# Optimization experiments

Hardware: AMD Instinct MI355X
Metric: run time of the kernel (lower is better)

Reference implementation:

```python
import jax, jax.numpy as jnp
import numpy as np

IN_F = 11008   # named 'in_features' in the module but used as the OUTPUT dim of F.linear
OUT_F = 4096   # named 'out_features' but is x's feature (input) dim
GROUP = 64


def dequantize_q40(w, s):
    """w: int8 (IN_F*OUT_F/GROUP/2, GROUP) packed nibbles; s: fp16 (IN_F*OUT_F/GROUP,).
    Matches torch: MSB = w >> 4 (arithmetic), LSB = w << 4 >> 4 (sign-extended low nibble).
    """
    msb = (w >> 4).astype(jnp.float16)                      # arithmetic shift on int8
    lsb = ((w & 15) - ((w & 8) << 1)).astype(jnp.float16)   # sign-extend low 4 bits to [-8, 7]
    q = jnp.concatenate([msb, lsb], axis=1).reshape(-1, GROUP)  # (n_groups, GROUP)
    fpval = (q * s[:, None]).astype(jnp.float16)
    return fpval.reshape(IN_F, OUT_F)


def setup_inputs() -> dict:
    key = jax.random.key(0)
    k1, k2, k3 = jax.random.split(key, 3)
    x = jax.random.normal(k1, (4, 2048, OUT_F), dtype=jnp.float16)
    n_rows = IN_F * OUT_F // GROUP // 2
    w = jax.random.randint(k2, (n_rows, GROUP), -128, 128, dtype=jnp.int32).astype(jnp.int8)
    s = (jax.random.uniform(k3, (IN_F * OUT_F // GROUP,), dtype=jnp.float32) * 0.02 + 0.001).astype(jnp.float16)
    return {"x": x, "w": w, "s": s}


def reference(x, w, s):
    # F.linear(x, deq) with deq of shape (IN_F, OUT_F): y = x @ deq.T
    deq = dequantize_q40(w, s)  # (IN_F, OUT_F) fp16
    return jnp.einsum('bsk,ok->bso', x, deq)  # (4, 2048, IN_F)
```

## Files before the change

kernel.cpp:

```cpp
#include <hip/hip_runtime.h>
#include <stdint.h>

#define M_DIM 8192
#define K_DIM 4096
#define N_DIM 11008

#define BM 128
#define BN 128
#define BK 64


typedef __attribute__((ext_vector_type(8))) _Float16 half8;
typedef __attribute__((ext_vector_type(4))) _Float16 half4;
typedef __attribute__((ext_vector_type(4))) float floatx4;

#define SWZ(row, col) ((col) ^ (((row) & 7) << 3))

__global__ __launch_bounds__(256) void dequant_q40(const int* __restrict__ w,
                                                   const float* __restrict__ s,
                                                   _Float16* __restrict__ deq) {
    int t = blockIdx.x * 256 + threadIdx.x;
    int r = t >> 3;
    int j = (t & 7) * 8;
    const int* wp = w + (size_t)r * 64 + j;
    int4 p0 = *(const int4*)(wp);
    int4 p1 = *(const int4*)(wp + 4);
    float sm = s[2 * r];
    float sl = s[2 * r + 1];
    int n = r >> 5, u = r & 31;
    _Float16* dm = deq + (size_t)n * K_DIM + u * 128 + j;
    int v[8] = {p0.x, p0.y, p0.z, p0.w, p1.x, p1.y, p1.z, p1.w};
    half8 vm, vl;
#pragma unroll
    for (int i = 0; i < 8; ++i) {
        int b = v[i];
        vm[i] = (_Float16)((float)(b >> 4) * sm);
        vl[i] = (_Float16)((float)((b << 28) >> 28) * sl);
    }
    *(half8*)dm = vm;
    *(half8*)(dm + 64) = vl;
}

__global__ __launch_bounds__(256, 2) void gemm_f16_bt(const float* __restrict__ A,
                                                      const _Float16* __restrict__ B,
                                                      float* __restrict__ C) {
    __shared__ _Float16 As[BM * BK];
    __shared__ _Float16 Bs[BN * BK];

    const int tid  = threadIdx.x;
    const int lane = tid & 63;
    const int wave = tid >> 6;
    const int wm = (wave >> 1) * 64;
    const int wn = (wave & 1) * 64;
    const int m0 = blockIdx.y * BM;
    const int n0 = blockIdx.x * BN;

    floatx4 acc[4][4] = {};
    const int lrow = lane & 15;
    const int quad = lane >> 4;
    const int kxor = (lrow & 7) << 3;

    for (int kk = 0; kk < K_DIM; kk += BK) {
        float4 av[8];
#pragma unroll
        for (int i = 0; i < 8; ++i) {
            int flat = i * 256 + tid;
            int row = flat >> 4;
            int col = (flat & 15) * 4;
            av[i] = *(const float4*)(A + (size_t)(m0 + row) * K_DIM + kk + col);
        }
        half8 bv[4];
#pragma unroll
        for (int i = 0; i < 4; ++i) {
            int flat = i * 256 + tid;
            int row = flat >> 3;
            int col = (flat & 7) * 8;
            bv[i] = *(const half8*)(B + (size_t)(n0 + row) * K_DIM + kk + col);
        }
        __syncthreads();
#pragma unroll
        for (int i = 0; i < 8; ++i) {
            int flat = i * 256 + tid;
            int row = flat >> 4;
            int col = (flat & 15) * 4;
            half4 a16;
            a16[0] = (_Float16)av[i].x;
            a16[1] = (_Float16)av[i].y;
            a16[2] = (_Float16)av[i].z;
            a16[3] = (_Float16)av[i].w;
            *(half4*)(As + row * BK + SWZ(row, col)) = a16;
        }
#pragma unroll
        for (int i = 0; i < 4; ++i) {
            int flat = i * 256 + tid;
            int row = flat >> 3;
            int col = (flat & 7) * 8;
            *(half8*)(Bs + row * BK + SWZ(row, col)) = bv[i];
        }
        __syncthreads();

#pragma unroll
        for (int ks = 0; ks < BK; ks += 32) {
            int koff = (ks + quad * 8) ^ kxor;
            half8 af[4], bf[4];
#pragma unroll
            for (int im = 0; im < 4; ++im)
                af[im] = *(const half8*)(As + (wm + im * 16 + lrow) * BK + koff);
#pragma unroll
            for (int in_ = 0; in_ < 4; ++in_)
                bf[in_] = *(const half8*)(Bs + (wn + in_ * 16 + lrow) * BK + koff);
#pragma unroll
            for (int im = 0; im < 4; ++im)
#pragma unroll
                for (int in_ = 0; in_ < 4; ++in_)
                    acc[im][in_] = __builtin_amdgcn_mfma_f32_16x16x32_f16(
                        af[im], bf[in_], acc[im][in_], 0, 0, 0);
        }
    }

#pragma unroll
    for (int im = 0; im < 4; ++im) {
#pragma unroll
        for (int in_ = 0; in_ < 4; ++in_) {
            int col = n0 + wn + in_ * 16 + lrow;
#pragma unroll
            for (int r = 0; r < 4; ++r) {
                int row = m0 + wm + im * 16 + quad * 4 + r;
                C[(size_t)row * N_DIM + col] = acc[im][in_][r];
            }
        }
    }
}

__global__ __launch_bounds__(256, 2) void gemm_fused(const float* __restrict__ A,
                                                     const int* __restrict__ W,
                                                     const float* __restrict__ S,
                                                     float* __restrict__ C) {
    __shared__ _Float16 As[BM * BK];
    __shared__ _Float16 Bs[BN * BK];

    const int tid  = threadIdx.x;
    const int lane = tid & 63;
    const int wave = tid >> 6;
    const int wm = (wave >> 1) * 64;
    const int wn = (wave & 1) * 64;
    const int m0 = blockIdx.y * BM;
    const int n0 = blockIdx.x * BN;

    floatx4 acc[4][4] = {};
    const int lrow = lane & 15;
    const int quad = lane >> 4;
    const int kxor = (lrow & 7) << 3;

    const int nn = tid >> 1;
    const int bh = (tid & 1) * 32;

    for (int kk = 0; kk < K_DIM; kk += BK) {
        float4 av[8];
#pragma unroll
        for (int i = 0; i < 8; ++i) {
            int flat = i * 256 + tid;
            int row = flat >> 4;
            int col = (flat & 15) * 4;
            av[i] = *(const float4*)(A + (size_t)(m0 + row) * K_DIM + kk + col);
        }
        int t64 = kk >> 6;
        int u = t64 >> 1;
        const int* wr = W + ((size_t)(n0 + nn) * 32 + u) * 64 + bh;
        float sc = S[(size_t)(n0 + nn) * 64 + t64];
        bool sel_lsb = (t64 & 1);
        half8 bq[4];
#pragma unroll
        for (int i8 = 0; i8 < 4; ++i8) {
            int4 pa = *(const int4*)(wr + i8 * 8);
            int4 pb = *(const int4*)(wr + i8 * 8 + 4);
            int vv[8] = {pa.x, pa.y, pa.z, pa.w, pb.x, pb.y, pb.z, pb.w};
#pragma unroll
            for (int q = 0; q < 8; ++q) {
                int b = vv[q];
                int qq = sel_lsb ? ((b << 28) >> 28) : (b >> 4);
                bq[i8][q] = (_Float16)((float)qq * sc);
            }
        }
        __syncthreads();
#pragma unroll
        for (int i = 0; i < 8; ++i) {
            int flat = i * 256 + tid;
            int row = flat >> 4;
            int col = (flat & 15) * 4;
            half4 a16;
            a16[0] = (_Float16)av[i].x;
            a16[1] = (_Float16)av[i].y;
            a16[2] = (_Float16)av[i].z;
            a16[3] = (_Float16)av[i].w;
            *(half4*)(As + row * BK + SWZ(row, col)) = a16;
        }
#pragma unroll
        for (int i8 = 0; i8 < 4; ++i8)
            *(half8*)(Bs + nn * BK + SWZ(nn, bh + i8 * 8)) = bq[i8];
        __syncthreads();

#pragma unroll
        for (int ks = 0; ks < BK; ks += 32) {
            int koff = (ks + quad * 8) ^ kxor;
            half8 af[4], bf[4];
#pragma unroll
            for (int im = 0; im < 4; ++im)
                af[im] = *(const half8*)(As + (wm + im * 16 + lrow) * BK + koff);
#pragma unroll
            for (int in_ = 0; in_ < 4; ++in_)
                bf[in_] = *(const half8*)(Bs + (wn + in_ * 16 + lrow) * BK + koff);
#pragma unroll
            for (int im = 0; im < 4; ++im)
#pragma unroll
                for (int in_ = 0; in_ < 4; ++in_)
                    acc[im][in_] = __builtin_amdgcn_mfma_f32_16x16x32_f16(
                        af[im], bf[in_], acc[im][in_], 0, 0, 0);
        }
    }

#pragma unroll
    for (int im = 0; im < 4; ++im) {
#pragma unroll
        for (int in_ = 0; in_ < 4; ++in_) {
            int col = n0 + wn + in_ * 16 + lrow;
#pragma unroll
            for (int r = 0; r < 4; ++r) {
                int row = m0 + wm + im * 16 + quad * 4 + r;
                C[(size_t)row * N_DIM + col] = acc[im][in_][r];
            }
        }
    }
}

extern "C" void kernel_launch(void* const* d_in, const int* in_sizes, int n_in,
                              void* d_out, int out_size, void* d_ws, size_t ws_size,
                              hipStream_t stream) {
    const float* x = (const float*)d_in[0];
    const int*   w = (const int*)d_in[1];
    const float* s = (const float*)d_in[2];
    float*     out = (float*)d_out;

    const size_t deq_bytes = (size_t)N_DIM * K_DIM * sizeof(_Float16);
    dim3 grid(N_DIM / BN, M_DIM / BM);

    if (ws_size >= deq_bytes) {
        _Float16* deq = (_Float16*)d_ws;
        dequant_q40<<<11008, 256, 0, stream>>>(w, s, deq);
        gemm_f16_bt<<<grid, 256, 0, stream>>>(x, deq, out);
    } else {
        gemm_fused<<<grid, 256, 0, stream>>>(x, w, s, out);
    }
}
```

Measured before the change: 1.581 ms.

## Pre-convert activations to fp16 and load GEMM tiles directly into LDS

Measured after the change: 1.324 ms. 16.3% less time.

```diff
diff --git a/kernel.cpp b/kernel.cpp
--- a/kernel.cpp
+++ b/kernel.cpp
@@ -15,6 +15,11 @@
 typedef __attribute__((ext_vector_type(4))) float floatx4;
 
 #define SWZ(row, col) ((col) ^ (((row) & 7) << 3))
+
+#define GLD_LDS16(gp, lp)                                                     \
+    __builtin_amdgcn_global_load_lds(                                         \
+        (const __attribute__((address_space(1))) uint32_t*)(gp),              \
+        (__attribute__((address_space(3))) uint32_t*)(lp), 16, 0, 0)
 
 __global__ __launch_bounds__(256) void dequant_q40(const int* __restrict__ w,
                                                    const float* __restrict__ s,
@@ -41,6 +46,94 @@
     *(half8*)(dm + 64) = vl;
 }
 
+__global__ __launch_bounds__(256) void conv_a16(const float* __restrict__ A,
+                                                _Float16* __restrict__ A16) {
+    size_t t = (size_t)blockIdx.x * 256 + threadIdx.x;
+    const float* p = A + t * 8;
+    float4 v0 = *(const float4*)(p);
+    float4 v1 = *(const float4*)(p + 4);
+    half8 h;
+    h[0] = (_Float16)v0.x; h[1] = (_Float16)v0.y;
+    h[2] = (_Float16)v0.z; h[3] = (_Float16)v0.w;
+    h[4] = (_Float16)v1.x; h[5] = (_Float16)v1.y;
+    h[6] = (_Float16)v1.z; h[7] = (_Float16)v1.w;
+    *(half8*)(A16 + t * 8) = h;
+}
+
+__global__ __launch_bounds__(256, 2) void gemm_lds16(const _Float16* __restrict__ A,
+                                                     const _Float16* __restrict__ B,
+                                                     float* __restrict__ C) {
+    __shared__ _Float16 As[BM * BK];
+    __shared__ _Float16 Bs[BN * BK];
+
+    const int tid  = threadIdx.x;
+    const int lane = tid & 63;
+    const int wave = tid >> 6;
+    const int wm = (wave >> 1) * 64;
+    const int wn = (wave & 1) * 64;
+
+    const int nwg_per_xcd = (N_DIM / BN) * (M_DIM / BM) / 8;
+    int bid = blockIdx.x;
+    int swz = (bid & 7) * nwg_per_xcd + (bid >> 3);
+    const int n0 = (swz % (N_DIM / BN)) * BN;
+    const int m0 = (swz / (N_DIM / BN)) * BM;
+
+    const int lrow8 = lane >> 3;
+    const int lcol  = ((lane & 7) * 8) ^ (lrow8 << 3);
+
+    const _Float16* aptr = A + (size_t)(m0 + wave * 32 + lrow8) * K_DIM + lcol;
+    const _Float16* bptr = B + (size_t)(n0 + wave * 32 + lrow8) * K_DIM + lcol;
+    _Float16* asl = As + (wave * 32) * BK;
+    _Float16* bsl = Bs + (wave * 32) * BK;
+
+    floatx4 acc[4][4] = {};
+    const int lrow = lane & 15;
+    const int quad = lane >> 4;
+    const int kxor = (lrow & 7) << 3;
+
+    for (int kk = 0; kk < K_DIM; kk += BK) {
+        __syncthreads();
+#pragma unroll
+        for (int i = 0; i < 4; ++i)
+            GLD_LDS16(aptr + (size_t)(i * 8) * K_DIM + kk, asl + i * 8 * BK);
+#pragma unroll
+        for (int i = 0; i < 4; ++i)
+            GLD_LDS16(bptr + (size_t)(i * 8) * K_DIM + kk, bsl + i * 8 * BK);
+        __syncthreads();
+
+#pragma unroll
+        for (int ks = 0; ks < BK; ks += 32) {
+            int koff = (ks + quad * 8) ^ kxor;
+            half8 af[4], bf[4];
+#pragma unroll
+            for (int im = 0; im < 4; ++im)
+                af[im] = *(const half8*)(As + (wm + im * 16 + lrow) * BK + koff);
+#pragma unroll
+            for (int in_ = 0; in_ < 4; ++in_)
+                bf[in_] = *(const half8*)(Bs + (wn + in_ * 16 + lrow) * BK + koff);
+#pragma unroll
+            for (int im = 0; im < 4; ++im)
+#pragma unroll
+                for (int in_ = 0; in_ < 4; ++in_)
+                    acc[im][in_] = __builtin_amdgcn_mfma_f32_16x16x32_f16(
+                        af[im], bf[in_], acc[im][in_], 0, 0, 0);
+        }
+    }
+
+#pragma unroll
+    for (int im = 0; im < 4; ++im) {
+#pragma unroll
+        for (int in_ = 0; in_ < 4; ++in_) {
+            int col = n0 + wn + in_ * 16 + lrow;
+#pragma unroll
+            for (int r = 0; r < 4; ++r) {
+                int row = m0 + wm + im * 16 + quad * 4 + r;
+                C[(size_t)row * N_DIM + col] = acc[im][in_][r];
+            }
+        }
+    }
+}
+
 __global__ __launch_bounds__(256, 2) void gemm_f16_bt(const float* __restrict__ A,
                                                       const _Float16* __restrict__ B,
                                                       float* __restrict__ C) {
@@ -242,13 +335,21 @@
     float*     out = (float*)d_out;
 
     const size_t deq_bytes = (size_t)N_DIM * K_DIM * sizeof(_Float16);
-    dim3 grid(N_DIM / BN, M_DIM / BM);
-
-    if (ws_size >= deq_bytes) {
+    const size_t a16_bytes = (size_t)M_DIM * K_DIM * sizeof(_Float16);
+
+    if (ws_size >= deq_bytes + a16_bytes) {
         _Float16* deq = (_Float16*)d_ws;
+        _Float16* a16 = (_Float16*)((char*)d_ws + deq_bytes);
+        dequant_q40<<<11008, 256, 0, stream>>>(w, s, deq);
+        conv_a16<<<(M_DIM * K_DIM / 8) / 256, 256, 0, stream>>>(x, a16);
+        gemm_lds16<<<(N_DIM / BN) * (M_DIM / BM), 256, 0, stream>>>(a16, deq, out);
+    } else if (ws_size >= deq_bytes) {
+        _Float16* deq = (_Float16*)d_ws;
+        dim3 grid(N_DIM / BN, M_DIM / BM);
         dequant_q40<<<11008, 256, 0, stream>>>(w, s, deq);
         gemm_f16_bt<<<grid, 256, 0, stream>>>(x, deq, out);
     } else {
+        dim3 grid(N_DIM / BN, M_DIM / BM);
         gemm_fused<<<grid, 256, 0, stream>>>(x, w, s, out);
     }
 }
```
